# Kernel optimization log

Measured on AMD Instinct MI355X. Metric: run time of the kernel, lower is better.

Reference implementation:

```python
import jax, jax.numpy as jnp
import numpy as np

TOPK = 10
NUM_CLASSES = 80
ALPHA = 0.5
BETA = 6.0
EPS = 1e-16


def _iou_xyxy(b1, b2):
    # b1, b2 broadcastable [..., 4] in xyxy; matches bbox_iou(xywh=False, CIoU=False)
    b1_x1, b1_y1, b1_x2, b1_y2 = b1[..., 0], b1[..., 1], b1[..., 2], b1[..., 3]
    b2_x1, b2_y1, b2_x2, b2_y2 = b2[..., 0], b2[..., 1], b2[..., 2], b2[..., 3]
    inter = jnp.clip(jnp.minimum(b1_x2, b2_x2) - jnp.maximum(b1_x1, b2_x1), 0) * \
            jnp.clip(jnp.minimum(b1_y2, b2_y2) - jnp.maximum(b1_y1, b2_y1), 0)
    w1, h1 = b1_x2 - b1_x1, b1_y2 - b1_y1 + EPS
    w2, h2 = b2_x2 - b2_x1, b2_y2 - b2_y1 + EPS
    union = w1 * h1 + w2 * h2 - inter + EPS
    return inter / union


def _assign_one(pd_s, pd_b, gt_l, gt_b, m, anc):
    # pd_s [A,C], pd_b [A,4], gt_l [N,1], gt_b [N,4], m [N,1] bool, anc [A,2]
    A = pd_s.shape[0]
    N = gt_l.shape[0]
    valid = m[:, 0]                                  # [N] padded-gt mask
    labels = gt_l[:, 0]                              # [N]
    scores = pd_s[:, labels]                         # [A,N] gather per-gt class score
    ious = _iou_xyxy(gt_b[None, :, :], pd_b[:, None, :])   # [A,N]
    align = scores ** ALPHA * ious ** BETA           # [A,N]
    # anchor-center-inside-gt test
    lt = anc[:, None, :] - gt_b[None, :, :2]         # [A,N,2]
    rb = gt_b[None, :, 2:] - anc[:, None, :]         # [A,N,2]
    in_gts = jnp.concatenate([lt, rb], axis=-1).min(axis=-1) > 0  # [A,N]
    amf = align * in_gts                             # align_metric_filter
    amf = jnp.where(valid[None, :], amf, 0.0)        # padded gts contribute nothing
    # top-k anchors per gt (over anchor dim)
    topk_idx = jax.lax.top_k(amf.T, TOPK)[1]         # [N,TOPK]
    mask_topk = jnp.zeros((N, A), dtype=bool).at[jnp.arange(N)[:, None], topk_idx].set(True).T  # [A,N]
    mask_pos = mask_topk & in_gts & valid[None, :]   # [A,N]
    fg = mask_pos.any(axis=1)                        # [A]
    # argmax over valid gts (padded columns pushed below any valid amf >= 0)
    amf_arg = jnp.where(valid[None, :], amf, -1.0)
    gt_idx = jnp.argmax(amf_arg, axis=1)             # [A]
    t_labels = jnp.where(fg, labels[gt_idx], NUM_CLASSES).astype(jnp.int32)
    t_bboxes = jnp.where(fg[:, None], gt_b[gt_idx], 0.0)
    am_max = jnp.clip(jnp.max(amf_arg, axis=1), 0.0)  # [A]
    BIG = jnp.float32(1e30)
    mn = jnp.min(jnp.where(fg, am_max, BIG))
    mx = jnp.max(jnp.where(fg, am_max, -BIG))
    norm = (am_max - mn) / (mx - mn + 1e-9)
    onehot = jax.nn.one_hot(t_labels, NUM_CLASSES, dtype=pd_s.dtype)  # label==C -> all-zero row
    t_scores = jnp.where(fg[:, None], onehot * norm[:, None], 0.0)
    return t_labels, t_bboxes, t_scores, fg


def setup_inputs() -> dict:
    key = jax.random.key(0)
    B, A, N, C = 32, 8400, 64, NUM_CLASSES
    ks = jax.random.split(key, 8)
    pd_scores = jax.random.uniform(ks[0], (B, A, C), dtype=jnp.float32)
    xy1 = jax.random.uniform(ks[1], (B, A, 2), dtype=jnp.float32) * 600.0
    wh = jax.random.uniform(ks[2], (B, A, 2), dtype=jnp.float32) * 60.0 + 4.0
    pd_bboxes = jnp.concatenate([xy1, xy1 + wh], axis=-1)
    anc_points = jax.random.uniform(ks[3], (A, 2), dtype=jnp.float32) * 640.0
    gxy1 = jax.random.uniform(ks[4], (B, N, 2), dtype=jnp.float32) * 500.0
    gwh = jax.random.uniform(ks[5], (B, N, 2), dtype=jnp.float32) * 140.0 + 20.0
    gt_bboxes = jnp.concatenate([gxy1, gxy1 + gwh], axis=-1)
    gt_labels = jax.random.randint(ks[6], (B, N, 1), 0, C, dtype=jnp.int32)
    counts = jax.random.randint(ks[7], (B,), 1, N + 1)
    mask_gt = (jnp.arange(N)[None, :] < counts[:, None])[..., None]  # [B,N,1] bool
    return {"pd_scores": pd_scores, "pd_bboxes": pd_bboxes, "anc_points": anc_points,
            "gt_labels": gt_labels, "gt_bboxes": gt_bboxes, "mask_gt": mask_gt}


def reference(pd_scores, pd_bboxes, anc_points, gt_labels, gt_bboxes, mask_gt):
    return jax.vmap(_assign_one, in_axes=(0, 0, 0, 0, 0, None))(
        pd_scores, pd_bboxes, gt_labels, gt_bboxes, mask_gt, anc_points)
```

## Files before the change

### kernel.cpp

```cpp
#include <hip/hip_runtime.h>

#define A_N 8400
#define B_N 32
#define NGT 64
#define NC  80
#define BA  (B_N * A_N)
#define NCOL (B_N * NGT)

__global__ __launch_bounds__(256) void k_init_all(int* __restrict__ fg,
                                                  int* __restrict__ cnts,
                                                  unsigned* __restrict__ mn_g,
                                                  unsigned* __restrict__ mx_g) {
  int idx = blockIdx.x * 256 + threadIdx.x;
  if (idx < BA) fg[idx] = 0;
  if (idx < NCOL) cnts[idx] = 0;
  if (idx < B_N) {
    mn_g[idx] = __float_as_uint(1e30f);
    mx_g[idx] = 0u;
  }
}

__global__ __launch_bounds__(256) void k_pairs(
    const float* __restrict__ pd_s, const float* __restrict__ pd_b,
    const float* __restrict__ anc, const int* __restrict__ gt_l,
    const float* __restrict__ gt_b, const int* __restrict__ mgt,
    unsigned long long* __restrict__ lists, int* __restrict__ cnts, int cap,
    int* __restrict__ gt_idx, float* __restrict__ am_max_g) {
#pragma clang fp contract(off)
  int b = blockIdx.y, tid = threadIdx.x;
  int a0 = blockIdx.x * 256, a = a0 + tid;
  bool av = a < A_N;

  __shared__ float4 gb_s[NGT];
  __shared__ int lab_s[NGT];
  __shared__ float4 pb_s[256];
  __shared__ float2 ap_s[256];
  __shared__ unsigned long long key_s[256];
  __shared__ unsigned short wl[256 * 32];
  __shared__ int wl_cnt;
  __shared__ int cnt_sh;

  if (tid < NGT) {
    gb_s[tid] = ((const float4*)gt_b)[b * NGT + tid];
    lab_s[tid] = gt_l[b * NGT + tid];
    unsigned long long m = __ballot(mgt[b * NGT + tid] != 0);
    if (tid == 0) cnt_sh = __popcll(m);
  }
  pb_s[tid] = av ? ((const float4*)pd_b)[(size_t)b * A_N + a]
                 : make_float4(0.f, 0.f, 0.f, 0.f);
  ap_s[tid] = av ? ((const float2*)anc)[a] : make_float2(-1e30f, -1e30f);
  key_s[tid] = 63ull;
  if (tid == 0) wl_cnt = 0;
  __syncthreads();
  int cnt = cnt_sh;
  float2 ap = ap_s[tid];

  for (int g0 = 0; g0 < cnt; g0 += 32) {
    int ge = (g0 + 32 < cnt) ? g0 + 32 : cnt;
    if (av) {
      for (int n = g0; n < ge; n++) {
        float4 gb = gb_s[n];
        float mn = fminf(fminf(ap.x - gb.x, ap.y - gb.y),
                         fminf(gb.z - ap.x, gb.w - ap.y));
        if (mn > 0.0f) {
          int p = atomicAdd(&wl_cnt, 1);
          wl[p] = (unsigned short)((tid << 6) | (n & 63));
        }
      }
    }
    __syncthreads();
    int m = wl_cnt;
    for (int i = tid; i < m; i += 256) {
      int e = wl[i];
      int al = e >> 6, n = e & 63;
      int ag = a0 + al;
      float4 gb = gb_s[n];
      float4 pb = pb_s[al];
      float iw = fmaxf(fminf(gb.z, pb.z) - fmaxf(gb.x, pb.x), 0.0f);
      float ih = fmaxf(fminf(gb.w, pb.w) - fmaxf(gb.y, pb.y), 0.0f);
      float inter = iw * ih;
      float w1 = gb.z - gb.x, h1 = (gb.w - gb.y) + 1e-16f;
      float w2 = pb.z - pb.x, h2 = (pb.w - pb.y) + 1e-16f;
      float uni = ((w1 * h1 + w2 * h2) - inter) + 1e-16f;
      float iou = inter / uni;
      float sc = pd_s[((size_t)b * A_N + ag) * NC + (size_t)lab_s[n]];
      float v = sqrtf(sc) * powf(iou, 6.0f);
      if (v > 0.0f) {
        unsigned vb = __float_as_uint(v);
        int col = b * NGT + n;
        int pos = atomicAdd(&cnts[col], 1);
        if (pos < cap) {
          lists[(size_t)col * cap + pos] =
              ((unsigned long long)vb << 32) |
              (unsigned long long)(0xFFFFFFFFu - (unsigned)ag);
        }
        atomicMax(&key_s[al],
                  ((unsigned long long)vb << 32) | (unsigned long long)(63 - n));
      }
    }
    __syncthreads();
    if (tid == 0) wl_cnt = 0;
    __syncthreads();
  }

  if (av) {
    unsigned long long k = key_s[tid];
    size_t i = (size_t)b * A_N + a;
    gt_idx[i] = 63 - (int)(k & 63ull);
    am_max_g[i] = __uint_as_float((unsigned)(k >> 32));
  }
}

__global__ __launch_bounds__(64) void k_topk_sparse(
    const unsigned long long* __restrict__ lists, const int* __restrict__ cnts,
    int cap, const int* __restrict__ mgt, const float* __restrict__ anc,
    const float* __restrict__ gt_b, const float* __restrict__ am_max_g,
    int* __restrict__ fg_mask, unsigned* __restrict__ mn_g,
    unsigned* __restrict__ mx_g) {
  int b = blockIdx.x, n = blockIdx.y, tid = threadIdx.x;
  if (mgt[b * NGT + n] == 0) return;
  int col = b * NGT + n;
  int P = cnts[col];
  if (P > cap) P = cap;
  const unsigned long long* list = lists + (size_t)col * cap;

  const unsigned MN_ID = __float_as_uint(1e30f);
  unsigned loc_mn = MN_ID, loc_mx = 0u;

  if (P >= 10) {
    unsigned long long top[10];
#pragma unroll
    for (int j = 0; j < 10; j++) top[j] = 0ull;
    for (int i = tid; i < P; i += 64) {
      unsigned long long key = list[i];
#pragma unroll
      for (int j = 0; j < 10; j++) {
        if (key > top[j]) { unsigned long long t = top[j]; top[j] = key; key = t; }
      }
    }
    for (int r = 0; r < 10; r++) {
      unsigned long long g = top[0];
#pragma unroll
      for (int off = 32; off >= 1; off >>= 1) {
        unsigned long long o = __shfl_xor(g, off, 64);
        g = (o > g) ? o : g;
      }
      if (top[0] == g) {
#pragma unroll
        for (int j = 0; j < 9; j++) top[j] = top[j + 1];
        top[9] = 0ull;
      }
      if (tid == r) {
        int a = (int)(0xFFFFFFFFu - (unsigned)(g & 0xFFFFFFFFull));
        atomicOr(&fg_mask[(size_t)b * A_N + a], 1);
        unsigned u = __float_as_uint(am_max_g[(size_t)b * A_N + a]);
        loc_mn = (u < loc_mn) ? u : loc_mn;
        loc_mx = (u > loc_mx) ? u : loc_mx;
      }
    }
#pragma unroll
    for (int off = 32; off >= 1; off >>= 1) {
      unsigned o1 = __shfl_xor(loc_mn, off, 64);
      loc_mn = (o1 < loc_mn) ? o1 : loc_mn;
      unsigned o2 = __shfl_xor(loc_mx, off, 64);
      loc_mx = (o2 > loc_mx) ? o2 : loc_mx;
    }
    if (tid == 0) {
      if (loc_mn != MN_ID) atomicMin(&mn_g[b], loc_mn);
      if (loc_mx != 0u || loc_mn != MN_ID) atomicMax(&mx_g[b], loc_mx);
    }
  } else if (tid == 0) {
    int pos_a[9];
    for (int i = 0; i < P; i++) {
      int a = (int)(0xFFFFFFFFu - (unsigned)(list[i] & 0xFFFFFFFFull));
      pos_a[i] = a;
      atomicOr(&fg_mask[(size_t)b * A_N + a], 1);
      unsigned u = __float_as_uint(am_max_g[(size_t)b * A_N + a]);
      loc_mn = (u < loc_mn) ? u : loc_mn;
      loc_mx = (u > loc_mx) ? u : loc_mx;
    }
    float4 gb = ((const float4*)gt_b)[b * NGT + n];
    int need = 10 - P;
    int a = 0;
    while (need > 0 && a < A_N) {
      bool is_pos = false;
      for (int i = 0; i < P; i++) is_pos |= (pos_a[i] == a);
      if (!is_pos) {
        float2 ap = ((const float2*)anc)[a];
        float mn = fminf(fminf(ap.x - gb.x, ap.y - gb.y),
                         fminf(gb.z - ap.x, gb.w - ap.y));
        if (mn > 0.0f) {
          atomicOr(&fg_mask[(size_t)b * A_N + a], 1);
          unsigned u = __float_as_uint(am_max_g[(size_t)b * A_N + a]);
          loc_mn = (u < loc_mn) ? u : loc_mn;
          loc_mx = (u > loc_mx) ? u : loc_mx;
        }
        need--;
      }
      a++;
    }
    if (loc_mn != MN_ID) atomicMin(&mn_g[b], loc_mn);
    if (loc_mx != 0u || loc_mn != MN_ID) atomicMax(&mx_g[b], loc_mx);
  }
}

__global__ __launch_bounds__(256) void k_out_fused(
    const int* __restrict__ gt_l, const float* __restrict__ gt_b,
    const int* __restrict__ fg_mask, const int* __restrict__ gt_idx,
    const float* __restrict__ am_max_g, const unsigned* __restrict__ mn_g,
    const unsigned* __restrict__ mx_g, float* __restrict__ out) {
  int b = blockIdx.y;
  int tid = threadIdx.x;
  int a0 = blockIdx.x * 256;
  int a = a0 + tid;

  __shared__ int cls_s[256];
  __shared__ float norm_s[256];

  if (a < A_N) {
    size_t i = (size_t)b * A_N + a;
    bool fg = fg_mask[i] != 0;
    int bi = gt_idx[i];
    float amx = am_max_g[i];
    float mn = __uint_as_float(mn_g[b]);
    float mx = __uint_as_float(mx_g[b]);
    float norm = (amx - mn) / ((mx - mn) + 1e-9f);
    int lab = gt_l[b * NGT + bi];

    out[i] = fg ? (float)lab : (float)NC;
    float4 bb = fg ? ((const float4*)gt_b)[b * NGT + bi]
                   : make_float4(0.f, 0.f, 0.f, 0.f);
    ((float4*)(out + BA))[i] = bb;
    out[(size_t)85 * BA + i] = fg ? 1.0f : 0.0f;
    cls_s[tid] = fg ? lab : -1;
    norm_s[tid] = fg ? norm : 0.0f;
  } else {
    cls_s[tid] = -1;
    norm_s[tid] = 0.0f;
  }
  __syncthreads();

  int nA = A_N - a0;
  if (nA > 256) nA = 256;
  float4* dst = (float4*)(out + (size_t)5 * BA + ((size_t)b * A_N + a0) * NC);
  int nvec = nA * (NC / 4);
  for (int t = tid; t < nvec; t += 256) {
    int al = t / (NC / 4);
    int c0 = (t - al * (NC / 4)) * 4;
    int cls = cls_s[al];
    float nv = norm_s[al];
    float4 r;
    r.x = (c0 == cls) ? nv : 0.0f;
    r.y = (c0 + 1 == cls) ? nv : 0.0f;
    r.z = (c0 + 2 == cls) ? nv : 0.0f;
    r.w = (c0 + 3 == cls) ? nv : 0.0f;
    dst[t] = r;
  }
}

extern "C" void kernel_launch(void* const* d_in, const int* in_sizes, int n_in,
                              void* d_out, int out_size, void* d_ws,
                              size_t ws_size, hipStream_t stream) {
  const float* pd_s = (const float*)d_in[0];
  const float* pd_b = (const float*)d_in[1];
  const float* anc  = (const float*)d_in[2];
  const int*   gt_l = (const int*)d_in[3];
  const float* gt_b = (const float*)d_in[4];
  const int*   mgt  = (const int*)d_in[5];

  float* out = (float*)d_out;
  char* ws = (char*)d_ws;

  const size_t SMALL = (size_t)BA * 4;
  size_t small_bytes = 3 * SMALL + (size_t)NCOL * 4 + 256;
  size_t avail = (ws_size > small_bytes) ? (ws_size - small_bytes) : 0;
  int cap = (int)(avail / ((size_t)NCOL * 8));
  if (cap > 4096) cap = 4096;
  if (cap < 1) cap = 1;

  unsigned long long* lists = (unsigned long long*)ws;
  char* sb = ws + (size_t)NCOL * 8 * cap;
  int*      fg_mask  = (int*)sb;
  int*      gt_idx   = (int*)(sb + SMALL);
  float*    am_max_g = (float*)(sb + 2 * SMALL);
  int*      cnts     = (int*)(sb + 3 * SMALL);
  unsigned* mn_g     = (unsigned*)(sb + 3 * SMALL + (size_t)NCOL * 4);
  unsigned* mx_g     = mn_g + B_N;

  dim3 g2((A_N + 255) / 256, B_N);
  k_init_all<<<(BA + 255) / 256, 256, 0, stream>>>(fg_mask, cnts, mn_g, mx_g);
  k_pairs<<<g2, 256, 0, stream>>>(pd_s, pd_b, anc, gt_l, gt_b, mgt, lists,
                                  cnts, cap, gt_idx, am_max_g);
  k_topk_sparse<<<dim3(B_N, NGT), 64, 0, stream>>>(lists, cnts, cap, mgt, anc,
                                                   gt_b, am_max_g, fg_mask,
                                                   mn_g, mx_g);
  k_out_fused<<<g2, 256, 0, stream>>>(gt_l, gt_b, fg_mask, gt_idx, am_max_g,
                                      mn_g, mx_g, out);
}
```

Measured before the change: 184.6 us.

## Pack per-anchor state into one 64-bit record and trim init and top-k paths

Per-anchor fg flag, best-gt index and max align metric are packed into a single 64-bit record, so k_pairs no longer needs a full fg_mask clear and k_out reads one array. The init kernel becomes a single tiny block, and k_pairs prefilters pairs whose boxes do not overlap before enqueueing them. The small-count top-k fallback is parallelised across the wave, assuming the needed filler anchors fall within the first 19 indices. Output writes use nontemporal stores. The fallback's bounded-window assumption changes semantics if filler anchors lie beyond index 18.

```diff
diff --git a/kernel.cpp b/kernel.cpp
--- a/kernel.cpp
+++ b/kernel.cpp
@@ -7,16 +7,16 @@
 #define BA  (B_N * A_N)
 #define NCOL (B_N * NGT)
 
-__global__ __launch_bounds__(256) void k_init_all(int* __restrict__ fg,
-                                                  int* __restrict__ cnts,
-                                                  unsigned* __restrict__ mn_g,
-                                                  unsigned* __restrict__ mx_g) {
-  int idx = blockIdx.x * 256 + threadIdx.x;
-  if (idx < BA) fg[idx] = 0;
-  if (idx < NCOL) cnts[idx] = 0;
-  if (idx < B_N) {
-    mn_g[idx] = __float_as_uint(1e30f);
-    mx_g[idx] = 0u;
+typedef float f4 __attribute__((ext_vector_type(4)));
+
+__global__ __launch_bounds__(256) void k_init(int* __restrict__ cnts,
+                                              unsigned* __restrict__ mn_g,
+                                              unsigned* __restrict__ mx_g) {
+  int tid = threadIdx.x;
+  for (int i = tid; i < NCOL; i += 256) cnts[i] = 0;
+  if (tid < B_N) {
+    mn_g[tid] = __float_as_uint(1e30f);
+    mx_g[tid] = 0u;
   }
 }
 
@@ -25,7 +25,7 @@
     const float* __restrict__ anc, const int* __restrict__ gt_l,
     const float* __restrict__ gt_b, const int* __restrict__ mgt,
     unsigned long long* __restrict__ lists, int* __restrict__ cnts, int cap,
-    int* __restrict__ gt_idx, float* __restrict__ am_max_g) {
+    unsigned long long* __restrict__ recs) {
 #pragma clang fp contract(off)
   int b = blockIdx.y, tid = threadIdx.x;
   int a0 = blockIdx.x * 256, a = a0 + tid;
@@ -34,7 +34,6 @@
   __shared__ float4 gb_s[NGT];
   __shared__ int lab_s[NGT];
   __shared__ float4 pb_s[256];
-  __shared__ float2 ap_s[256];
   __shared__ unsigned long long key_s[256];
   __shared__ unsigned short wl[256 * 32];
   __shared__ int wl_cnt;
@@ -46,14 +45,14 @@
     unsigned long long m = __ballot(mgt[b * NGT + tid] != 0);
     if (tid == 0) cnt_sh = __popcll(m);
   }
-  pb_s[tid] = av ? ((const float4*)pd_b)[(size_t)b * A_N + a]
+  float4 pb = av ? ((const float4*)pd_b)[(size_t)b * A_N + a]
                  : make_float4(0.f, 0.f, 0.f, 0.f);
-  ap_s[tid] = av ? ((const float2*)anc)[a] : make_float2(-1e30f, -1e30f);
-  key_s[tid] = 63ull;
+  float2 ap = av ? ((const float2*)anc)[a] : make_float2(-1e30f, -1e30f);
+  pb_s[tid] = pb;
+  key_s[tid] = (unsigned long long)(63 << 1);
   if (tid == 0) wl_cnt = 0;
   __syncthreads();
   int cnt = cnt_sh;
-  float2 ap = ap_s[tid];
 
   for (int g0 = 0; g0 < cnt; g0 += 32) {
     int ge = (g0 + 32 < cnt) ? g0 + 32 : cnt;
@@ -62,7 +61,9 @@
         float4 gb = gb_s[n];
         float mn = fminf(fminf(ap.x - gb.x, ap.y - gb.y),
                          fminf(gb.z - ap.x, gb.w - ap.y));
-        if (mn > 0.0f) {
+        float iwr = fminf(gb.z, pb.z) - fmaxf(gb.x, pb.x);
+        float ihr = fminf(gb.w, pb.w) - fmaxf(gb.y, pb.y);
+        if (mn > 0.0f && iwr > 0.0f && ihr > 0.0f) {
           int p = atomicAdd(&wl_cnt, 1);
           wl[p] = (unsigned short)((tid << 6) | (n & 63));
         }
@@ -75,12 +76,12 @@
       int al = e >> 6, n = e & 63;
       int ag = a0 + al;
       float4 gb = gb_s[n];
-      float4 pb = pb_s[al];
-      float iw = fmaxf(fminf(gb.z, pb.z) - fmaxf(gb.x, pb.x), 0.0f);
-      float ih = fmaxf(fminf(gb.w, pb.w) - fmaxf(gb.y, pb.y), 0.0f);
+      float4 pbl = pb_s[al];
+      float iw = fmaxf(fminf(gb.z, pbl.z) - fmaxf(gb.x, pbl.x), 0.0f);
+      float ih = fmaxf(fminf(gb.w, pbl.w) - fmaxf(gb.y, pbl.y), 0.0f);
       float inter = iw * ih;
       float w1 = gb.z - gb.x, h1 = (gb.w - gb.y) + 1e-16f;
-      float w2 = pb.z - pb.x, h2 = (pb.w - pb.y) + 1e-16f;
+      float w2 = pbl.z - pbl.x, h2 = (pbl.w - pbl.y) + 1e-16f;
       float uni = ((w1 * h1 + w2 * h2) - inter) + 1e-16f;
       float iou = inter / uni;
       float sc = pd_s[((size_t)b * A_N + ag) * NC + (size_t)lab_s[n]];
@@ -94,8 +95,8 @@
               ((unsigned long long)vb << 32) |
               (unsigned long long)(0xFFFFFFFFu - (unsigned)ag);
         }
-        atomicMax(&key_s[al],
-                  ((unsigned long long)vb << 32) | (unsigned long long)(63 - n));
+        atomicMax(&key_s[al], ((unsigned long long)vb << 32) |
+                                  (unsigned long long)((63 - n) << 1));
       }
     }
     __syncthreads();
@@ -103,26 +104,21 @@
     __syncthreads();
   }
 
-  if (av) {
-    unsigned long long k = key_s[tid];
-    size_t i = (size_t)b * A_N + a;
-    gt_idx[i] = 63 - (int)(k & 63ull);
-    am_max_g[i] = __uint_as_float((unsigned)(k >> 32));
-  }
-}
-
-__global__ __launch_bounds__(64) void k_topk_sparse(
+  if (av) recs[(size_t)b * A_N + a] = key_s[tid];
+}
+
+__global__ __launch_bounds__(64) void k_topk(
     const unsigned long long* __restrict__ lists, const int* __restrict__ cnts,
     int cap, const int* __restrict__ mgt, const float* __restrict__ anc,
-    const float* __restrict__ gt_b, const float* __restrict__ am_max_g,
-    int* __restrict__ fg_mask, unsigned* __restrict__ mn_g,
-    unsigned* __restrict__ mx_g) {
+    const float* __restrict__ gt_b, unsigned long long* __restrict__ recs,
+    unsigned* __restrict__ mn_g, unsigned* __restrict__ mx_g) {
   int b = blockIdx.x, n = blockIdx.y, tid = threadIdx.x;
   if (mgt[b * NGT + n] == 0) return;
   int col = b * NGT + n;
   int P = cnts[col];
   if (P > cap) P = cap;
   const unsigned long long* list = lists + (size_t)col * cap;
+  unsigned* recw = (unsigned*)recs;
 
   const unsigned MN_ID = __float_as_uint(1e30f);
   unsigned loc_mn = MN_ID, loc_mx = 0u;
@@ -151,64 +147,66 @@
         top[9] = 0ull;
       }
       if (tid == r) {
-        int a = (int)(0xFFFFFFFFu - (unsigned)(g & 0xFFFFFFFFull));
-        atomicOr(&fg_mask[(size_t)b * A_N + a], 1);
-        unsigned u = __float_as_uint(am_max_g[(size_t)b * A_N + a]);
+        size_t idx = (size_t)b * A_N +
+                     (size_t)(0xFFFFFFFFu - (unsigned)(g & 0xFFFFFFFFull));
+        atomicOr(&recw[2 * idx], 1u);
+        unsigned u = recw[2 * idx + 1];
         loc_mn = (u < loc_mn) ? u : loc_mn;
         loc_mx = (u > loc_mx) ? u : loc_mx;
       }
     }
-#pragma unroll
-    for (int off = 32; off >= 1; off >>= 1) {
-      unsigned o1 = __shfl_xor(loc_mn, off, 64);
-      loc_mn = (o1 < loc_mn) ? o1 : loc_mn;
-      unsigned o2 = __shfl_xor(loc_mx, off, 64);
-      loc_mx = (o2 > loc_mx) ? o2 : loc_mx;
-    }
-    if (tid == 0) {
-      if (loc_mn != MN_ID) atomicMin(&mn_g[b], loc_mn);
-      if (loc_mx != 0u || loc_mn != MN_ID) atomicMax(&mx_g[b], loc_mx);
-    }
-  } else if (tid == 0) {
-    int pos_a[9];
-    for (int i = 0; i < P; i++) {
-      int a = (int)(0xFFFFFFFFu - (unsigned)(list[i] & 0xFFFFFFFFull));
-      pos_a[i] = a;
-      atomicOr(&fg_mask[(size_t)b * A_N + a], 1);
-      unsigned u = __float_as_uint(am_max_g[(size_t)b * A_N + a]);
+  } else {
+    int my_a = -1;
+    if (tid < P)
+      my_a = (int)(0xFFFFFFFFu - (unsigned)(list[tid] & 0xFFFFFFFFull));
+    if (tid < P) {
+      size_t idx = (size_t)b * A_N + my_a;
+      atomicOr(&recw[2 * idx], 1u);
+      unsigned u = recw[2 * idx + 1];
       loc_mn = (u < loc_mn) ? u : loc_mn;
       loc_mx = (u > loc_mx) ? u : loc_mx;
     }
-    float4 gb = ((const float4*)gt_b)[b * NGT + n];
-    int need = 10 - P;
-    int a = 0;
-    while (need > 0 && a < A_N) {
-      bool is_pos = false;
-      for (int i = 0; i < P; i++) is_pos |= (pos_a[i] == a);
-      if (!is_pos) {
-        float2 ap = ((const float2*)anc)[a];
-        float mn = fminf(fminf(ap.x - gb.x, ap.y - gb.y),
-                         fminf(gb.z - ap.x, gb.w - ap.y));
-        if (mn > 0.0f) {
-          atomicOr(&fg_mask[(size_t)b * A_N + a], 1);
-          unsigned u = __float_as_uint(am_max_g[(size_t)b * A_N + a]);
-          loc_mn = (u < loc_mn) ? u : loc_mn;
-          loc_mx = (u > loc_mx) ? u : loc_mx;
-        }
-        need--;
-      }
-      a++;
-    }
-    if (loc_mn != MN_ID) atomicMin(&mn_g[b], loc_mn);
-    if (loc_mx != 0u || loc_mn != MN_ID) atomicMax(&mx_g[b], loc_mx);
-  }
-}
-
-__global__ __launch_bounds__(256) void k_out_fused(
+    bool is_pos = false;
+    for (int i = 0; i < P; i++) {
+      int ai = __shfl(my_a, i, 64);
+      is_pos |= (ai == tid);
+    }
+    bool cand = (tid < 19) && !is_pos;
+    unsigned long long fm = __ballot(cand);
+    int rank = __popcll(fm & ((1ull << tid) - 1ull));
+    if (cand && rank < 10 - P) {
+      float4 gb = ((const float4*)gt_b)[b * NGT + n];
+      float2 ap = ((const float2*)anc)[tid];
+      float mn = fminf(fminf(ap.x - gb.x, ap.y - gb.y),
+                       fminf(gb.z - ap.x, gb.w - ap.y));
+      if (mn > 0.0f) {
+        size_t idx = (size_t)b * A_N + tid;
+        atomicOr(&recw[2 * idx], 1u);
+        unsigned u = recw[2 * idx + 1];
+        loc_mn = (u < loc_mn) ? u : loc_mn;
+        loc_mx = (u > loc_mx) ? u : loc_mx;
+      }
+    }
+  }
+
+#pragma unroll
+  for (int off = 32; off >= 1; off >>= 1) {
+    unsigned o1 = __shfl_xor(loc_mn, off, 64);
+    loc_mn = (o1 < loc_mn) ? o1 : loc_mn;
+    unsigned o2 = __shfl_xor(loc_mx, off, 64);
+    loc_mx = (o2 > loc_mx) ? o2 : loc_mx;
+  }
+  if (tid == 0 && loc_mn != MN_ID) {
+    atomicMin(&mn_g[b], loc_mn);
+    atomicMax(&mx_g[b], loc_mx);
+  }
+}
+
+__global__ __launch_bounds__(256) void k_out(
     const int* __restrict__ gt_l, const float* __restrict__ gt_b,
-    const int* __restrict__ fg_mask, const int* __restrict__ gt_idx,
-    const float* __restrict__ am_max_g, const unsigned* __restrict__ mn_g,
-    const unsigned* __restrict__ mx_g, float* __restrict__ out) {
+    const unsigned long long* __restrict__ recs,
+    const unsigned* __restrict__ mn_g, const unsigned* __restrict__ mx_g,
+    float* __restrict__ out) {
   int b = blockIdx.y;
   int tid = threadIdx.x;
   int a0 = blockIdx.x * 256;
@@ -219,19 +217,25 @@
 
   if (a < A_N) {
     size_t i = (size_t)b * A_N + a;
-    bool fg = fg_mask[i] != 0;
-    int bi = gt_idx[i];
-    float amx = am_max_g[i];
+    unsigned long long rec = recs[i];
+    bool fg = (rec & 1ull) != 0;
+    int bi = 63 - (int)((rec >> 1) & 63ull);
+    float amx = __uint_as_float((unsigned)(rec >> 32));
     float mn = __uint_as_float(mn_g[b]);
     float mx = __uint_as_float(mx_g[b]);
     float norm = (amx - mn) / ((mx - mn) + 1e-9f);
     int lab = gt_l[b * NGT + bi];
 
-    out[i] = fg ? (float)lab : (float)NC;
-    float4 bb = fg ? ((const float4*)gt_b)[b * NGT + bi]
-                   : make_float4(0.f, 0.f, 0.f, 0.f);
-    ((float4*)(out + BA))[i] = bb;
-    out[(size_t)85 * BA + i] = fg ? 1.0f : 0.0f;
+    __builtin_nontemporal_store(fg ? (float)lab : (float)NC, &out[i]);
+    f4 bb;
+    if (fg) {
+      float4 t = ((const float4*)gt_b)[b * NGT + bi];
+      bb.x = t.x; bb.y = t.y; bb.z = t.z; bb.w = t.w;
+    } else {
+      bb = (f4){0.f, 0.f, 0.f, 0.f};
+    }
+    __builtin_nontemporal_store(bb, &((f4*)(out + BA))[i]);
+    __builtin_nontemporal_store(fg ? 1.0f : 0.0f, &out[(size_t)85 * BA + i]);
     cls_s[tid] = fg ? lab : -1;
     norm_s[tid] = fg ? norm : 0.0f;
   } else {
@@ -242,19 +246,19 @@
 
   int nA = A_N - a0;
   if (nA > 256) nA = 256;
-  float4* dst = (float4*)(out + (size_t)5 * BA + ((size_t)b * A_N + a0) * NC);
+  f4* dst = (f4*)(out + (size_t)5 * BA + ((size_t)b * A_N + a0) * NC);
   int nvec = nA * (NC / 4);
   for (int t = tid; t < nvec; t += 256) {
     int al = t / (NC / 4);
     int c0 = (t - al * (NC / 4)) * 4;
     int cls = cls_s[al];
     float nv = norm_s[al];
-    float4 r;
+    f4 r;
     r.x = (c0 == cls) ? nv : 0.0f;
     r.y = (c0 + 1 == cls) ? nv : 0.0f;
     r.z = (c0 + 2 == cls) ? nv : 0.0f;
     r.w = (c0 + 3 == cls) ? nv : 0.0f;
-    dst[t] = r;
+    __builtin_nontemporal_store(r, &dst[t]);
   }
 }
 
@@ -271,8 +275,8 @@
   float* out = (float*)d_out;
   char* ws = (char*)d_ws;
 
-  const size_t SMALL = (size_t)BA * 4;
-  size_t small_bytes = 3 * SMALL + (size_t)NCOL * 4 + 256;
+  const size_t REC_BYTES = (size_t)BA * 8;
+  size_t small_bytes = REC_BYTES + (size_t)NCOL * 4 + 256;
   size_t avail = (ws_size > small_bytes) ? (ws_size - small_bytes) : 0;
   int cap = (int)(avail / ((size_t)NCOL * 8));
   if (cap > 4096) cap = 4096;
@@ -280,20 +284,16 @@
 
   unsigned long long* lists = (unsigned long long*)ws;
   char* sb = ws + (size_t)NCOL * 8 * cap;
-  int*      fg_mask  = (int*)sb;
-  int*      gt_idx   = (int*)(sb + SMALL);
-  float*    am_max_g = (float*)(sb + 2 * SMALL);
-  int*      cnts     = (int*)(sb + 3 * SMALL);
-  unsigned* mn_g     = (unsigned*)(sb + 3 * SMALL + (size_t)NCOL * 4);
-  unsigned* mx_g     = mn_g + B_N;
+  unsigned long long* recs = (unsigned long long*)sb;
+  int*      cnts = (int*)(sb + REC_BYTES);
+  unsigned* mn_g = (unsigned*)(sb + REC_BYTES + (size_t)NCOL * 4);
+  unsigned* mx_g = mn_g + B_N;
 
   dim3 g2((A_N + 255) / 256, B_N);
-  k_init_all<<<(BA + 255) / 256, 256, 0, stream>>>(fg_mask, cnts, mn_g, mx_g);
+  k_init<<<1, 256, 0, stream>>>(cnts, mn_g, mx_g);
   k_pairs<<<g2, 256, 0, stream>>>(pd_s, pd_b, anc, gt_l, gt_b, mgt, lists,
-                                  cnts, cap, gt_idx, am_max_g);
-  k_topk_sparse<<<dim3(B_N, NGT), 64, 0, stream>>>(lists, cnts, cap, mgt, anc,
-                                                   gt_b, am_max_g, fg_mask,
-                                                   mn_g, mx_g);
-  k_out_fused<<<g2, 256, 0, stream>>>(gt_l, gt_b, fg_mask, gt_idx, am_max_g,
-                                      mn_g, mx_g, out);
-}
+                                  cnts, cap, recs);
+  k_topk<<<dim3(B_N, NGT), 64, 0, stream>>>(lists, cnts, cap, mgt, anc, gt_b,
+                                            recs, mn_g, mx_g);
+  k_out<<<g2, 256, 0, stream>>>(gt_l, gt_b, recs, mn_g, mx_g, out);
+}
```

New measurement: 185.4 us. About the same (+0.4%).
